# Kernel tuning notes

Measured on AMD Instinct MI355X. Metric: run time of the kernel, lower is better.

## Reference

```python
import jax, jax.numpy as jnp
import numpy as np

IN_FEATURES = 4096
OUT_FEATURES = 4096
NNZ = 838860
BATCH = 512


def setup_inputs() -> dict:
    key = jax.random.key(0)
    kx, kr, kc, kv, kb = jax.random.split(key, 5)
    x = jax.random.normal(kx, (BATCH, IN_FEATURES), dtype=jnp.float32)
    row_idx = jax.random.randint(kr, (NNZ,), 0, OUT_FEATURES, dtype=jnp.int64)
    col_idx = jax.random.randint(kc, (NNZ,), 0, IN_FEATURES, dtype=jnp.int64)
    values = jax.random.normal(kv, (NNZ,), dtype=jnp.float32)
    bias = jax.random.normal(kb, (OUT_FEATURES,), dtype=jnp.float32)
    return {"x": x, "row_idx": row_idx, "col_idx": col_idx,
            "values": values, "bias": bias}


def reference(x, row_idx, col_idx, values, bias):
    # COO sparse linear: y[b, row] += x[b, col] * val, then add bias.
    x_flat = x.reshape(-1, IN_FEATURES)                    # [B, in]
    weighted = x_flat[:, col_idx] * values                 # [B, nnz]
    out = jnp.zeros((x_flat.shape[0], OUT_FEATURES), dtype=x.dtype)
    out = out.at[:, row_idx].add(weighted)                 # scatter-add per row
    out = out + bias
    return out.reshape(x.shape[:-1] + (OUT_FEATURES,))
```

## Files before the change

### kernel.cpp

```cpp
#include <hip/hip_runtime.h>

#define IN_F    4096
#define OUT_F   4096
#define K_DIM   4096
#define NNZ_C   838860
#define BATCH   512
#define SPLITK  4
#define KS      (K_DIM / SPLITK)
#define BK      32
#define BM      128
#define BN      128

typedef short bf16x8 __attribute__((ext_vector_type(8)));
typedef float f32x4  __attribute__((ext_vector_type(4)));

__device__ __forceinline__ unsigned short f2bf(float f) {
    unsigned u = __float_as_uint(f);
    u += 0x7fffu + ((u >> 16) & 1u);
    return (unsigned short)(u >> 16);
}
__device__ __forceinline__ void gload_lds16(const void* g, void* l) {
    __builtin_amdgcn_global_load_lds(
        (const __attribute__((address_space(1))) unsigned int*)g,
        (__attribute__((address_space(3))) unsigned int*)l, 16, 0, 0);
}

__global__ void convert_x(const float* __restrict__ x,
                          unsigned short* __restrict__ xb) {
    int i = blockIdx.x * 256 + threadIdx.x;
    const float4* p = (const float4*)x + (size_t)i * 2;
    float4 a = p[0], b = p[1];
    union { unsigned short h[8]; bf16x8 v; } u;
    u.h[0] = f2bf(a.x); u.h[1] = f2bf(a.y); u.h[2] = f2bf(a.z); u.h[3] = f2bf(a.w);
    u.h[4] = f2bf(b.x); u.h[5] = f2bf(b.y); u.h[6] = f2bf(b.z); u.h[7] = f2bf(b.w);
    ((bf16x8*)xb)[i] = u.v;
}

__global__ void scatter_pk(const int* __restrict__ row_idx,
                           const int* __restrict__ col_idx,
                           const float* __restrict__ values,
                           unsigned short* __restrict__ W) {
    int i = blockIdx.x * 256 + threadIdx.x;
    if (i >= NNZ_C) return;
    unsigned idx = (unsigned)row_idx[i] * K_DIM + (unsigned)col_idx[i];
    unsigned short h = f2bf(values[i]);
    unsigned data = (idx & 1u) ? ((unsigned)h << 16) : (unsigned)h;
    unsigned long long addr = (unsigned long long)(W + (idx & ~1u));
    asm volatile("global_atomic_pk_add_bf16 %0, %1, off"
                 :: "v"(addr), "v"(data) : "memory");
}

__global__ void init_out_bias(const float* __restrict__ bias,
                              float* __restrict__ out) {
    int i = blockIdx.x * 256 + threadIdx.x;
    float4 b = ((const float4*)bias)[i & (OUT_F / 4 - 1)];
    ((float4*)out)[i] = b;
}

__global__ void __launch_bounds__(256)
gemm_bt(const unsigned short* __restrict__ Abf,
        const unsigned short* __restrict__ Wbf,
        float* __restrict__ out) {
    __shared__ __align__(16) unsigned short As[BM * BK];
    __shared__ __align__(16) unsigned short Bs[BN * BK];

    const int nt = blockIdx.x, mt = blockIdx.y, s = blockIdx.z;
    const int t = threadIdx.x, w = t >> 6, ln = t & 63;
    const int wm = w & 1, wn = w >> 1;
    const int ks0 = s * KS;

    const int srow = w * 16 + (ln >> 2);
    const int scol = (((ln & 3) ^ ((ln >> 3) & 3)) * 8);
    const unsigned short* gA0 = Abf + (size_t)(mt * BM + srow) * K_DIM + ks0 + scol;
    const unsigned short* gA1 = gA0 + (size_t)64 * K_DIM;
    const unsigned short* gB0 = Wbf + (size_t)(nt * BN + srow) * K_DIM + ks0 + scol;
    const unsigned short* gB1 = gB0 + (size_t)64 * K_DIM;
    unsigned short* lA0 = &As[(w * 16) * BK];
    unsigned short* lA1 = &As[(64 + w * 16) * BK];
    unsigned short* lB0 = &Bs[(w * 16) * BK];
    unsigned short* lB1 = &Bs[(64 + w * 16) * BK];

    const int quad = ln >> 4, lanem = ln & 15;
    const int rsw = (quad ^ ((lanem >> 1) & 3)) * 8;
    const unsigned short* rA = &As[(wm * 64 + lanem) * BK + rsw];
    const unsigned short* rB = &Bs[(wn * 64 + lanem) * BK + rsw];

    f32x4 acc[4][4];
#pragma unroll
    for (int mi = 0; mi < 4; ++mi)
#pragma unroll
        for (int ni = 0; ni < 4; ++ni)
            acc[mi][ni] = (f32x4){0.f, 0.f, 0.f, 0.f};

    for (int kt = 0; kt < KS / BK; ++kt) {
        __syncthreads();
        gload_lds16(gA0 + kt * BK, lA0);
        gload_lds16(gA1 + kt * BK, lA1);
        gload_lds16(gB0 + kt * BK, lB0);
        gload_lds16(gB1 + kt * BK, lB1);
        __syncthreads();

        bf16x8 af[4], bfr[4];
#pragma unroll
        for (int mi = 0; mi < 4; ++mi) af[mi]  = *(const bf16x8*)(rA + mi * 16 * BK);
#pragma unroll
        for (int ni = 0; ni < 4; ++ni) bfr[ni] = *(const bf16x8*)(rB + ni * 16 * BK);
#pragma unroll
        for (int mi = 0; mi < 4; ++mi)
#pragma unroll
            for (int ni = 0; ni < 4; ++ni)
                acc[mi][ni] = __builtin_amdgcn_mfma_f32_16x16x32_bf16(
                    af[mi], bfr[ni], acc[mi][ni], 0, 0, 0);
    }

    const int row0 = mt * BM + wm * 64 + quad * 4;
    const int col0 = nt * BN + wn * 64 + lanem;
#pragma unroll
    for (int mi = 0; mi < 4; ++mi)
#pragma unroll
        for (int ni = 0; ni < 4; ++ni) {
            int c = col0 + ni * 16;
#pragma unroll
            for (int r = 0; r < 4; ++r) {
                size_t o = (size_t)(row0 + mi * 16 + r) * OUT_F + c;
                atomicAdd(&out[o], acc[mi][ni][r]);
            }
        }
}

extern "C" void kernel_launch(void* const* d_in, const int* in_sizes, int n_in,
                              void* d_out, int out_size, void* d_ws, size_t ws_size,
                              hipStream_t stream) {
    const float* x       = (const float*)d_in[0];
    const int*   row_idx = (const int*)d_in[1];
    const int*   col_idx = (const int*)d_in[2];
    const float* values  = (const float*)d_in[3];
    const float* bias    = (const float*)d_in[4];
    float*       out     = (float*)d_out;

    unsigned short* xb = (unsigned short*)d_ws;
    unsigned short* W  = xb + (size_t)BATCH * K_DIM;

    hipMemsetAsync(W, 0, (size_t)OUT_F * K_DIM * 2, stream);
    convert_x<<<1024, 256, 0, stream>>>(x, xb);
    scatter_pk<<<(NNZ_C + 255) / 256, 256, 0, stream>>>(row_idx, col_idx, values, W);
    init_out_bias<<<2048, 256, 0, stream>>>(bias, out);
    gemm_bt<<<dim3(OUT_F / BN, BATCH / BM, SPLITK), 256, 0, stream>>>(xb, W, out);
}
```

Before: 172.4 us.

## Fuse prep kernels, vectorize scatter, and replace split-K atomics with partial buffers

Merges the W zeroing, the x conversion to bf16 and the bias init into one prep kernel, which removes the memset and two launches. The scatter kernel now handles four nonzeros per thread using vector loads. When the workspace is large enough, the GEMM uses split-K of 8, with each slice writing plain stores into its own partial buffer and bias folded into slice 0, and a separate reduce kernel sums the parts. This replaces fp32 atomics on the output but adds about 56 MB of partial-buffer traffic and an extra launch.

```diff
diff --git a/kernel.cpp b/kernel.cpp
--- a/kernel.cpp
+++ b/kernel.cpp
@@ -5,8 +5,6 @@
 #define K_DIM   4096
 #define NNZ_C   838860
 #define BATCH   512
-#define SPLITK  4
-#define KS      (K_DIM / SPLITK)
 #define BK      32
 #define BM      128
 #define BN      128
@@ -25,49 +23,71 @@
         (__attribute__((address_space(3))) unsigned int*)l, 16, 0, 0);
 }
 
-__global__ void convert_x(const float* __restrict__ x,
-                          unsigned short* __restrict__ xb) {
+#define N_WZ   (OUT_F * K_DIM / 8)
+#define N_CVT  (BATCH * K_DIM / 8)
+#define N_OUT  (BATCH * OUT_F / 4)
+__global__ void prep(const float* __restrict__ x,
+                     unsigned short* __restrict__ xb,
+                     const float* __restrict__ bias,
+                     float* __restrict__ out,
+                     uint4* __restrict__ Wz, int do_bias) {
     int i = blockIdx.x * 256 + threadIdx.x;
-    const float4* p = (const float4*)x + (size_t)i * 2;
-    float4 a = p[0], b = p[1];
-    union { unsigned short h[8]; bf16x8 v; } u;
-    u.h[0] = f2bf(a.x); u.h[1] = f2bf(a.y); u.h[2] = f2bf(a.z); u.h[3] = f2bf(a.w);
-    u.h[4] = f2bf(b.x); u.h[5] = f2bf(b.y); u.h[6] = f2bf(b.z); u.h[7] = f2bf(b.w);
-    ((bf16x8*)xb)[i] = u.v;
-}
+    if (i < N_WZ) { Wz[i] = make_uint4(0, 0, 0, 0); return; }
+    i -= N_WZ;
+    if (i < N_CVT) {
+        const float4* p = (const float4*)x + (size_t)i * 2;
+        float4 a = p[0], b = p[1];
+        union { unsigned short h[8]; bf16x8 v; } u;
+        u.h[0] = f2bf(a.x); u.h[1] = f2bf(a.y); u.h[2] = f2bf(a.z); u.h[3] = f2bf(a.w);
+        u.h[4] = f2bf(b.x); u.h[5] = f2bf(b.y); u.h[6] = f2bf(b.z); u.h[7] = f2bf(b.w);
+        ((bf16x8*)xb)[i] = u.v;
+        return;
+    }
+    i -= N_CVT;
+    if (i < N_OUT && do_bias) {
+        float4 b = ((const float4*)bias)[i & (OUT_F / 4 - 1)];
+        ((float4*)out)[i] = b;
+    }
+}
+#define PREP_BLOCKS ((N_WZ + N_CVT + N_OUT) / 256)
 
 __global__ void scatter_pk(const int* __restrict__ row_idx,
                            const int* __restrict__ col_idx,
                            const float* __restrict__ values,
                            unsigned short* __restrict__ W) {
     int i = blockIdx.x * 256 + threadIdx.x;
-    if (i >= NNZ_C) return;
-    unsigned idx = (unsigned)row_idx[i] * K_DIM + (unsigned)col_idx[i];
-    unsigned short h = f2bf(values[i]);
-    unsigned data = (idx & 1u) ? ((unsigned)h << 16) : (unsigned)h;
-    unsigned long long addr = (unsigned long long)(W + (idx & ~1u));
-    asm volatile("global_atomic_pk_add_bf16 %0, %1, off"
-                 :: "v"(addr), "v"(data) : "memory");
-}
-
-__global__ void init_out_bias(const float* __restrict__ bias,
-                              float* __restrict__ out) {
-    int i = blockIdx.x * 256 + threadIdx.x;
-    float4 b = ((const float4*)bias)[i & (OUT_F / 4 - 1)];
-    ((float4*)out)[i] = b;
-}
-
+    if (i >= NNZ_C / 4) return;
+    int4   r4 = ((const int4*)row_idx)[i];
+    int4   c4 = ((const int4*)col_idx)[i];
+    float4 v4 = ((const float4*)values)[i];
+#pragma unroll
+    for (int j = 0; j < 4; ++j) {
+        int r = (&r4.x)[j], c = (&c4.x)[j];
+        float v = (&v4.x)[j];
+        unsigned idx = (unsigned)r * K_DIM + (unsigned)c;
+        unsigned short h = f2bf(v);
+        unsigned data = (idx & 1u) ? ((unsigned)h << 16) : (unsigned)h;
+        unsigned long long addr = (unsigned long long)(W + (idx & ~1u));
+        asm volatile("global_atomic_pk_add_bf16 %0, %1, off"
+                     :: "v"(addr), "v"(data) : "memory");
+    }
+}
+
+template <int EPI, int SK>
 __global__ void __launch_bounds__(256)
 gemm_bt(const unsigned short* __restrict__ Abf,
         const unsigned short* __restrict__ Wbf,
-        float* __restrict__ out) {
+        const float* __restrict__ bias,
+        float* __restrict__ out,
+        float* __restrict__ parts) {
     __shared__ __align__(16) unsigned short As[BM * BK];
     __shared__ __align__(16) unsigned short Bs[BN * BK];
 
     const int nt = blockIdx.x, mt = blockIdx.y, s = blockIdx.z;
     const int t = threadIdx.x, w = t >> 6, ln = t & 63;
     const int wm = w & 1, wn = w >> 1;
-    const int ks0 = s * KS;
+    const int KSs = K_DIM / SK;
+    const int ks0 = s * KSs;
 
     const int srow = w * 16 + (ln >> 2);
     const int scol = (((ln & 3) ^ ((ln >> 3) & 3)) * 8);
@@ -92,7 +112,7 @@
         for (int ni = 0; ni < 4; ++ni)
             acc[mi][ni] = (f32x4){0.f, 0.f, 0.f, 0.f};
 
-    for (int kt = 0; kt < KS / BK; ++kt) {
+    for (int kt = 0; kt < KSs / BK; ++kt) {
         __syncthreads();
         gload_lds16(gA0 + kt * BK, lA0);
         gload_lds16(gA1 + kt * BK, lA1);
@@ -115,17 +135,41 @@
 
     const int row0 = mt * BM + wm * 64 + quad * 4;
     const int col0 = nt * BN + wn * 64 + lanem;
-#pragma unroll
-    for (int mi = 0; mi < 4; ++mi)
-#pragma unroll
-        for (int ni = 0; ni < 4; ++ni) {
-            int c = col0 + ni * 16;
-#pragma unroll
-            for (int r = 0; r < 4; ++r) {
-                size_t o = (size_t)(row0 + mi * 16 + r) * OUT_F + c;
-                atomicAdd(&out[o], acc[mi][ni][r]);
-            }
-        }
+    if (EPI == 0) {
+        float bv[4];
+#pragma unroll
+        for (int ni = 0; ni < 4; ++ni) bv[ni] = (s == 0) ? bias[col0 + ni * 16] : 0.f;
+        float* dst = (s == 0) ? out : parts + (size_t)(s - 1) * BATCH * OUT_F;
+#pragma unroll
+        for (int mi = 0; mi < 4; ++mi)
+#pragma unroll
+            for (int ni = 0; ni < 4; ++ni)
+#pragma unroll
+                for (int r = 0; r < 4; ++r)
+                    dst[(size_t)(row0 + mi * 16 + r) * OUT_F + col0 + ni * 16] =
+                        acc[mi][ni][r] + bv[ni];
+    } else {
+#pragma unroll
+        for (int mi = 0; mi < 4; ++mi)
+#pragma unroll
+            for (int ni = 0; ni < 4; ++ni)
+#pragma unroll
+                for (int r = 0; r < 4; ++r)
+                    atomicAdd(&out[(size_t)(row0 + mi * 16 + r) * OUT_F + col0 + ni * 16],
+                              acc[mi][ni][r]);
+    }
+}
+
+__global__ void reduce_parts(float* __restrict__ out,
+                             const float* __restrict__ parts) {
+    int i = blockIdx.x * 256 + threadIdx.x;
+    float4 a = ((const float4*)out)[i];
+#pragma unroll
+    for (int p = 0; p < 7; ++p) {
+        float4 b = ((const float4*)(parts + (size_t)p * BATCH * OUT_F))[i];
+        a.x += b.x; a.y += b.y; a.z += b.z; a.w += b.w;
+    }
+    ((float4*)out)[i] = a;
 }
 
 extern "C" void kernel_launch(void* const* d_in, const int* in_sizes, int n_in,
@@ -140,10 +184,22 @@
 
     unsigned short* xb = (unsigned short*)d_ws;
     unsigned short* W  = xb + (size_t)BATCH * K_DIM;
-
-    hipMemsetAsync(W, 0, (size_t)OUT_F * K_DIM * 2, stream);
-    convert_x<<<1024, 256, 0, stream>>>(x, xb);
-    scatter_pk<<<(NNZ_C + 255) / 256, 256, 0, stream>>>(row_idx, col_idx, values, W);
-    init_out_bias<<<2048, 256, 0, stream>>>(bias, out);
-    gemm_bt<<<dim3(OUT_F / BN, BATCH / BM, SPLITK), 256, 0, stream>>>(xb, W, out);
-}
+    float* parts = (float*)(W + (size_t)OUT_F * K_DIM);
+    size_t need = (size_t)BATCH * K_DIM * 2 + (size_t)OUT_F * K_DIM * 2
+                + (size_t)7 * BATCH * OUT_F * 4;
+    bool use_parts = (ws_size >= need);
+
+    prep<<<PREP_BLOCKS, 256, 0, stream>>>(x, xb, bias, out, (uint4*)W,
+                                          use_parts ? 0 : 1);
+    scatter_pk<<<(NNZ_C / 4 + 255) / 256, 256, 0, stream>>>(
+        row_idx, col_idx, values, W);
+
+    if (use_parts) {
+        gemm_bt<0, 8><<<dim3(OUT_F / BN, BATCH / BM, 8), 256, 0, stream>>>(
+            xb, W, bias, out, parts);
+        reduce_parts<<<BATCH * OUT_F / 4 / 256, 256, 0, stream>>>(out, parts);
+    } else {
+        gemm_bt<1, 4><<<dim3(OUT_F / BN, BATCH / BM, 4), 256, 0, stream>>>(
+            xb, W, bias, out, nullptr);
+    }
+}
```

Measured after the change: 163.0 us. 1.06x faster.
